# Kernel tuning notes

Hardware: AMD Instinct MI355X
Metric: run time of the kernel (lower is better)

The kernel has to match this reference:

```python
import jax, jax.numpy as jnp
import numpy as np

N = 40000       # nodes
E = 512000      # edges (avg degree 16)
D = 128         # embed_dim
H = 128         # hidden_dim
R = 8           # num_relations
B = 8           # num_bases
C = 3           # output classes (hardcoded in conv7)


def _prelu(x, a):
    # torch.nn.PReLU(num_parameters=C): per-channel slope
    return jnp.where(x >= 0, x, a * x)


def _rgcn(x, src, dst, etype, bases, comp, root, bias):
    """PyG RGCNConv with basis decomposition, aggr='mean' (default).
    out[i] = sum_r mean_{e: dst=i, type=r} (W_r @ x[src_e]) + root @ x[i] + bias
    W_r = sum_b comp[r,b] * bases[b]. Aggregation is linear, so we aggregate
    source features per (node, relation) first, then apply W_r once per node.
    """
    n = x.shape[0]
    seg = dst * R + etype                      # composite (node, relation) id
    gx = x[src]                                # [E, in]  (big gather)
    agg = jax.ops.segment_sum(gx, seg, num_segments=n * R)              # [N*R, in]
    cnt = jax.ops.segment_sum(jnp.ones((src.shape[0],), x.dtype), seg,
                              num_segments=n * R)                        # [N*R]
    agg = agg / jnp.maximum(cnt, 1.0)[:, None]                           # mean per (node, rel)
    agg = agg.reshape(n, R, -1)                                          # [N, R, in]
    Wr = jnp.einsum('rb,bio->rio', comp, bases)                          # [R, in, out]
    return jnp.einsum('nri,rio->no', agg, Wr) + x @ root + bias


def setup_inputs() -> dict:
    key = jax.random.key(0)
    ks = jax.random.split(key, 20)
    num_x = jax.random.normal(ks[0], (N, 1), jnp.float32)
    x = jax.random.normal(ks[1], (N, D), jnp.float32)
    edge_index = jax.random.randint(ks[2], (2, E), 0, N, jnp.int32)
    edge_type = jax.random.randint(ks[3], (E,), 0, R, jnp.int32)
    # params
    lin_w = jax.random.normal(ks[4], (1, D), jnp.float32) * 0.1
    lin_b = jax.random.normal(ks[5], (D,), jnp.float32) * 0.1
    prelu_a = 0.25 + 0.01 * jax.random.normal(ks[6], (7, D), jnp.float32)
    s = 1.0 / np.sqrt(H)
    bases = jax.random.normal(ks[7], (6, B, H, H), jnp.float32) * s   # conv1..conv6 (in==out==H)
    comp = jax.random.normal(ks[8], (6, R, B), jnp.float32) * (1.0 / np.sqrt(B))
    root = jax.random.normal(ks[9], (6, H, H), jnp.float32) * s
    bias = jax.random.normal(ks[10], (6, H), jnp.float32) * 0.1
    bases7 = jax.random.normal(ks[11], (B, H, C), jnp.float32) * s
    comp7 = jax.random.normal(ks[12], (R, B), jnp.float32) * (1.0 / np.sqrt(B))
    root7 = jax.random.normal(ks[13], (H, C), jnp.float32) * s
    bias7 = jax.random.normal(ks[14], (C,), jnp.float32) * 0.1
    return dict(num_x=num_x, x=x, edge_index=edge_index, edge_type=edge_type,
                lin_w=lin_w, lin_b=lin_b, prelu_a=prelu_a,
                bases=bases, comp=comp, root=root, bias=bias,
                bases7=bases7, comp7=comp7, root7=root7, bias7=bias7)


def reference(num_x, x, edge_index, edge_type, lin_w, lin_b, prelu_a,
              bases, comp, root, bias, bases7, comp7, root7, bias7):
    src, dst = edge_index[0], edge_index[1]
    h = _prelu(num_x @ lin_w + lin_b, prelu_a[0])   # act_lin(num_lin(num_x))
    h = h + x
    for i in range(6):  # conv1..conv6 + PReLU (dropout is identity in eval)
        h = _rgcn(h, src, dst, edge_type, bases[i], comp[i], root[i], bias[i])
        h = _prelu(h, prelu_a[i + 1])
    h = _rgcn(h, src, dst, edge_type, bases7, comp7, root7, bias7)  # conv7 -> 3 classes
    return jax.nn.log_softmax(h, axis=1)
```

## Files before the change

### kernel.cpp

```cpp
#include <hip/hip_runtime.h>

typedef unsigned short ushortT;
typedef ushortT ushort8 __attribute__((ext_vector_type(8)));
typedef short bf16x8 __attribute__((ext_vector_type(8)));
typedef float f32x4 __attribute__((ext_vector_type(4)));

#define NN 40000
#define NE 512000
#define DD 128
#define RR 8
#define NSEG (NN * RR)
#define KT 1152
#define NB_SCAN 1250

__device__ __forceinline__ float bf2f(ushortT u) { return __uint_as_float(((unsigned)u) << 16); }
__device__ __forceinline__ ushortT f2bf(float f) {
  unsigned u = __float_as_uint(f);
  unsigned r = (u + 0x7fffu + ((u >> 16) & 1u)) >> 16;
  return (ushortT)r;
}

__global__ void count_kernel(const int* __restrict__ dst, const int* __restrict__ et,
                             int* __restrict__ cnt) {
  int e = blockIdx.x * 256 + threadIdx.x;
  if (e < NE) atomicAdd(&cnt[dst[e] * RR + et[e]], 1);
}

__global__ void scan1_kernel(const int* __restrict__ cnt, int* __restrict__ offs,
                             int* __restrict__ bsum) {
  __shared__ int s[256];
  int tid = threadIdx.x, gid = blockIdx.x * 256 + tid;
  int v = cnt[gid];
  s[tid] = v; __syncthreads();
  for (int o = 1; o < 256; o <<= 1) {
    int t = (tid >= o) ? s[tid - o] : 0;
    __syncthreads(); s[tid] += t; __syncthreads();
  }
  offs[gid] = s[tid] - v;
  if (tid == 255) bsum[blockIdx.x] = s[255];
}

__global__ void scan2_kernel(int* __restrict__ bsum) {
  __shared__ int s[256];
  __shared__ int carry, tot;
  int tid = threadIdx.x;
  if (tid == 0) carry = 0;
  __syncthreads();
  for (int base = 0; base < NB_SCAN; base += 256) {
    int i = base + tid;
    int v = (i < NB_SCAN) ? bsum[i] : 0;
    s[tid] = v; __syncthreads();
    for (int o = 1; o < 256; o <<= 1) {
      int t = (tid >= o) ? s[tid - o] : 0;
      __syncthreads(); s[tid] += t; __syncthreads();
    }
    if (i < NB_SCAN) bsum[i] = s[tid] - v + carry;
    if (tid == 255) tot = s[255];
    __syncthreads();
    if (tid == 0) carry += tot;
    __syncthreads();
  }
}

__global__ void scan3_kernel(int* __restrict__ offs, const int* __restrict__ bsum,
                             const int* __restrict__ cnt, int* __restrict__ cursor) {
  int gid = blockIdx.x * 256 + threadIdx.x;
  int v = offs[gid] + bsum[blockIdx.x];
  offs[gid] = v;
  cursor[gid] = v;
  if (gid == NSEG - 1) offs[NSEG] = v + cnt[gid];
}

__global__ void fill_kernel(const int* __restrict__ src, const int* __restrict__ dst,
                            const int* __restrict__ et, int* __restrict__ cursor,
                            int* __restrict__ srcs) {
  int e = blockIdx.x * 256 + threadIdx.x;
  if (e >= NE) return;
  int seg = dst[e] * RR + et[e];
  int slot = atomicAdd(&cursor[seg], 1);
  srcs[slot] = src[e];
}

__global__ void init_h_kernel(const float* __restrict__ num_x, const float* __restrict__ x,
                              const float* __restrict__ lin_w, const float* __restrict__ lin_b,
                              const float* __restrict__ a0, ushortT* __restrict__ h) {
  int idx = blockIdx.x * 256 + threadIdx.x;
  if (idx >= NN * DD) return;
  int n = idx >> 7, d = idx & 127;
  float v = fmaf(num_x[n], lin_w[d], lin_b[d]);
  v = v >= 0.f ? v : a0[d] * v;
  h[idx] = f2bf(v + x[idx]);
}

__global__ void build_w_kernel(const float* __restrict__ bases, const float* __restrict__ comp,
                               const float* __restrict__ root, ushortT* __restrict__ Wt) {
  int idx = blockIdx.x * 256 + threadIdx.x;
  if (idx >= DD * KT) return;
  int j = idx / KT, k = idx - j * KT;
  float s;
  if (k < RR * DD) {
    int r = k >> 7, i = k & 127;
    s = 0.f;
#pragma unroll
    for (int b = 0; b < 8; ++b) s += comp[r * 8 + b] * bases[(b * DD + i) * DD + j];
  } else {
    s = root[(k - RR * DD) * DD + j];
  }
  Wt[idx] = f2bf(s);
}

__global__ __launch_bounds__(256)
void agg_kernel(const int* __restrict__ offs, const int* __restrict__ srcs,
                const ushortT* __restrict__ h, ushortT* __restrict__ Xagg) {
  int seg = blockIdx.x * 16 + (threadIdx.x >> 4);
  int l = threadIdx.x & 15;
  int beg = offs[seg], end = offs[seg + 1];
  float a[8] = {0.f, 0.f, 0.f, 0.f, 0.f, 0.f, 0.f, 0.f};
  int e = beg;
  for (; e + 2 <= end; e += 2) {
    int s0 = srcs[e], s1 = srcs[e + 1];
    ushort8 v0 = *(const ushort8*)&h[(size_t)s0 * DD + l * 8];
    ushort8 v1 = *(const ushort8*)&h[(size_t)s1 * DD + l * 8];
#pragma unroll
    for (int j = 0; j < 8; ++j) a[j] += bf2f(v0[j]) + bf2f(v1[j]);
  }
  if (e < end) {
    int s0 = srcs[e];
    ushort8 v0 = *(const ushort8*)&h[(size_t)s0 * DD + l * 8];
#pragma unroll
    for (int j = 0; j < 8; ++j) a[j] += bf2f(v0[j]);
  }
  float inv = (end > beg) ? 1.0f / (float)(end - beg) : 1.0f;
  ushort8 r;
#pragma unroll
  for (int j = 0; j < 8; ++j) r[j] = f2bf(a[j] * inv);
  *(ushort8*)&Xagg[(size_t)seg * DD + l * 8] = r;
}

__global__ __launch_bounds__(256)
void gemm_kernel(const ushortT* __restrict__ Xagg, const ushortT* __restrict__ h,
                 const ushortT* __restrict__ Wt, const float* __restrict__ bias,
                 const float* __restrict__ slope, ushortT* __restrict__ hout) {
  __shared__ ushortT As[64 * 64];
  __shared__ ushortT Bs[128 * 64];
  int tid = threadIdx.x, lane = tid & 63, wv = tid >> 6;
  int wr = wv >> 1, wc = wv & 1;
  int n0 = blockIdx.x * 64;
  int l8 = lane >> 3;
  int lp = lane & 7;
  f32x4 acc[2][4];
#pragma unroll
  for (int m = 0; m < 2; ++m)
#pragma unroll
    for (int n = 0; n < 4; ++n) acc[m][n] = (f32x4){0.f, 0.f, 0.f, 0.f};

  for (int kc = 0; kc < KT; kc += 64) {
#pragma unroll
    for (int j = 0; j < 2; ++j) {
      int row = wv * 16 + j * 8 + l8;
      int p = lp ^ (row & 7);
      const ushortT* g;
      if (kc < RR * DD) g = Xagg + (size_t)(n0 + row) * 1024 + kc + p * 8;
      else              g = h + (size_t)(n0 + row) * DD + (kc - RR * DD) + p * 8;
      __builtin_amdgcn_global_load_lds(
          (const __attribute__((address_space(1))) void*)g,
          (__attribute__((address_space(3))) void*)&As[(wv * 16 + j * 8) * 64], 16, 0, 0);
    }
#pragma unroll
    for (int j = 0; j < 4; ++j) {
      int col = wv * 32 + j * 8 + l8;
      int p = lp ^ (col & 7);
      const ushortT* g = Wt + (size_t)col * KT + kc + p * 8;
      __builtin_amdgcn_global_load_lds(
          (const __attribute__((address_space(1))) void*)g,
          (__attribute__((address_space(3))) void*)&Bs[(wv * 32 + j * 8) * 64], 16, 0, 0);
    }
    __syncthreads();
#pragma unroll
    for (int kk = 0; kk < 2; ++kk) {
      int ko2 = kk * 64 + (lane >> 4) * 16;
      bf16x8 a[2], b[4];
#pragma unroll
      for (int m = 0; m < 2; ++m) {
        int row = wr * 32 + m * 16 + (lane & 15);
        int off = ((row << 7) + ko2) ^ ((row & 7) << 4);
        a[m] = *(const bf16x8*)((const char*)As + off);
      }
#pragma unroll
      for (int n = 0; n < 4; ++n) {
        int col = wc * 64 + n * 16 + (lane & 15);
        int off = ((col << 7) + ko2) ^ ((col & 7) << 4);
        b[n] = *(const bf16x8*)((const char*)Bs + off);
      }
#pragma unroll
      for (int m = 0; m < 2; ++m)
#pragma unroll
        for (int n = 0; n < 4; ++n)
          acc[m][n] = __builtin_amdgcn_mfma_f32_16x16x32_bf16(a[m], b[n], acc[m][n], 0, 0, 0);
    }
    __syncthreads();
  }
#pragma unroll
  for (int m = 0; m < 2; ++m) {
    int row = n0 + wr * 32 + m * 16 + (lane >> 4) * 4;
#pragma unroll
    for (int n = 0; n < 4; ++n) {
      int col = wc * 64 + n * 16 + (lane & 15);
      float bcol = bias[col], scol = slope[col];
#pragma unroll
      for (int q = 0; q < 4; ++q) {
        float v = acc[m][n][q] + bcol;
        v = v >= 0.f ? v : scol * v;
        hout[(size_t)(row + q) * DD + col] = f2bf(v);
      }
    }
  }
}

__global__ void build_w7_kernel(const float* __restrict__ bases7, const float* __restrict__ comp7,
                                const float* __restrict__ root7, float* __restrict__ W7) {
  int idx = blockIdx.x * 256 + threadIdx.x;
  if (idx >= KT * 3) return;
  int row = idx / 3, c = idx - row * 3;
  if (row < RR * DD) {
    int r = row >> 7, i = row & 127;
    float s = 0.f;
#pragma unroll
    for (int b = 0; b < 8; ++b) s += comp7[r * 8 + b] * bases7[(b * DD + i) * 3 + c];
    W7[idx] = s;
  } else {
    W7[idx] = root7[(row - RR * DD) * 3 + c];
  }
}

__global__ void conv7_kernel(const ushortT* __restrict__ Xagg, const ushortT* __restrict__ h,
                             const float* __restrict__ W7, const float* __restrict__ bias7,
                             float* __restrict__ out) {
  int gw = (blockIdx.x * 256 + threadIdx.x) >> 6;
  if (gw >= NN) return;
  int lane = threadIdx.x & 63;
  float a0 = 0.f, a1 = 0.f, a2 = 0.f;
#pragma unroll
  for (int i = 0; i < 2; ++i) {
    int k0 = i * 512 + lane * 8;
    ushort8 v = *(const ushort8*)&Xagg[(size_t)gw * 1024 + k0];
#pragma unroll
    for (int j = 0; j < 8; ++j) {
      float xx = bf2f(v[j]);
      const float* w = &W7[(k0 + j) * 3];
      a0 = fmaf(xx, w[0], a0); a1 = fmaf(xx, w[1], a1); a2 = fmaf(xx, w[2], a2);
    }
  }
  {
    unsigned v = *(const unsigned*)&h[gw * DD + lane * 2];
    float x0 = __uint_as_float(v << 16), x1 = __uint_as_float(v & 0xffff0000u);
    int k0 = 1024 + lane * 2;
    const float* w0 = &W7[k0 * 3];
    const float* w1 = &W7[(k0 + 1) * 3];
    a0 = fmaf(x0, w0[0], a0); a1 = fmaf(x0, w0[1], a1); a2 = fmaf(x0, w0[2], a2);
    a0 = fmaf(x1, w1[0], a0); a1 = fmaf(x1, w1[1], a1); a2 = fmaf(x1, w1[2], a2);
  }
#pragma unroll
  for (int o = 32; o > 0; o >>= 1) {
    a0 += __shfl_down(a0, o);
    a1 += __shfl_down(a1, o);
    a2 += __shfl_down(a2, o);
  }
  if (lane == 0) {
    float l0 = a0 + bias7[0], l1 = a1 + bias7[1], l2 = a2 + bias7[2];
    float m = fmaxf(l0, fmaxf(l1, l2));
    float lse = m + logf(expf(l0 - m) + expf(l1 - m) + expf(l2 - m));
    out[gw * 3 + 0] = l0 - lse;
    out[gw * 3 + 1] = l1 - lse;
    out[gw * 3 + 2] = l2 - lse;
  }
}

extern "C" void kernel_launch(void* const* d_in, const int* in_sizes, int n_in,
                              void* d_out, int out_size, void* d_ws, size_t ws_size,
                              hipStream_t stream) {
  const float* num_x  = (const float*)d_in[0];
  const float* x      = (const float*)d_in[1];
  const int*   eidx   = (const int*)d_in[2];
  const int*   etype  = (const int*)d_in[3];
  const float* lin_w  = (const float*)d_in[4];
  const float* lin_b  = (const float*)d_in[5];
  const float* prelu  = (const float*)d_in[6];
  const float* bases  = (const float*)d_in[7];
  const float* comp   = (const float*)d_in[8];
  const float* root   = (const float*)d_in[9];
  const float* bias   = (const float*)d_in[10];
  const float* bases7 = (const float*)d_in[11];
  const float* comp7  = (const float*)d_in[12];
  const float* root7  = (const float*)d_in[13];
  const float* bias7  = (const float*)d_in[14];
  const int* srcv = eidx;
  const int* dstv = eidx + NE;
  float* out = (float*)d_out;

  char* p = (char*)d_ws;
  auto alloc = [&](size_t bytes) { char* q = p; p += (bytes + 255) & ~(size_t)255; return q; };
  int*     counts = (int*)alloc((size_t)NSEG * 4);
  int*     offs   = (int*)alloc((size_t)(NSEG + 1) * 4);
  int*     cursor = (int*)alloc((size_t)NSEG * 4);
  int*     bsum   = (int*)alloc((size_t)NB_SCAN * 4);
  int*     srcs   = (int*)alloc((size_t)NE * 4);
  ushortT* h0     = (ushortT*)alloc((size_t)NN * DD * 2);
  ushortT* h1     = (ushortT*)alloc((size_t)NN * DD * 2);
  ushortT* Xagg   = (ushortT*)alloc((size_t)NN * 1024 * 2);
  ushortT* Wt     = (ushortT*)alloc((size_t)DD * KT * 2);
  float*   W7     = (float*)alloc((size_t)KT * 3 * 4);
  if (ws_size < (size_t)(p - (char*)d_ws)) return;

  hipMemsetAsync(counts, 0, (size_t)NSEG * 4, stream);
  count_kernel<<<NE / 256, 256, 0, stream>>>(dstv, etype, counts);
  scan1_kernel<<<NB_SCAN, 256, 0, stream>>>(counts, offs, bsum);
  scan2_kernel<<<1, 256, 0, stream>>>(bsum);
  scan3_kernel<<<NB_SCAN, 256, 0, stream>>>(offs, bsum, counts, cursor);
  fill_kernel<<<NE / 256, 256, 0, stream>>>(srcv, dstv, etype, cursor, srcs);

  init_h_kernel<<<(NN * DD + 255) / 256, 256, 0, stream>>>(num_x, x, lin_w, lin_b, prelu, h0);

  ushortT* hin = h0;
  ushortT* hout = h1;
  for (int layer = 0; layer < 6; ++layer) {
    build_w_kernel<<<(DD * KT + 255) / 256, 256, 0, stream>>>(
        bases + (size_t)layer * 8 * DD * DD, comp + layer * RR * 8,
        root + (size_t)layer * DD * DD, Wt);
    agg_kernel<<<NSEG / 16, 256, 0, stream>>>(offs, srcs, hin, Xagg);
    gemm_kernel<<<NN / 64, 256, 0, stream>>>(Xagg, hin, Wt, bias + layer * DD,
                                             prelu + (layer + 1) * DD, hout);
    ushortT* t = hin; hin = hout; hout = t;
  }
  build_w7_kernel<<<(KT * 3 + 255) / 256, 256, 0, stream>>>(bases7, comp7, root7, W7);
  agg_kernel<<<NSEG / 16, 256, 0, stream>>>(offs, srcs, hin, Xagg);
  conv7_kernel<<<NN / 4, 256, 0, stream>>>(Xagg, hin, W7, bias7, out);
}
```

Before: 508.0 us.

## Fuse neighbor aggregation into RGCN GEMM and drop Xagg buffer

Each layer's aggregation is now done inside the GEMM block: for each relation, threads gather and average neighbor rows straight into an LDS A-tile, then run MFMA against the matching weight slab. This removes the 80MB Xagg write and read per layer. Conv7 also aggregates inline, and all six weight builds are batched into one launch before the loop. In exchange the gather has less parallelism (4 threads per node, serial per-edge loop, 500 blocks), and there is no overlap between gather latency and MFMA.

```diff
diff --git a/kernel.cpp b/kernel.cpp
--- a/kernel.cpp
+++ b/kernel.cpp
@@ -4,6 +4,8 @@
 typedef ushortT ushort8 __attribute__((ext_vector_type(8)));
 typedef short bf16x8 __attribute__((ext_vector_type(8)));
 typedef float f32x4 __attribute__((ext_vector_type(4)));
+typedef unsigned int uint32;
+typedef uint32 uint32x4 __attribute__((ext_vector_type(4)));
 
 #define NN 40000
 #define NE 512000
@@ -12,6 +14,7 @@
 #define NSEG (NN * RR)
 #define KT 1152
 #define NB_SCAN 1250
+#define ECAP 1536
 
 __device__ __forceinline__ float bf2f(ushortT u) { return __uint_as_float(((unsigned)u) << 16); }
 __device__ __forceinline__ ushortT f2bf(float f) {
@@ -93,111 +96,129 @@
 }
 
 __global__ void build_w_kernel(const float* __restrict__ bases, const float* __restrict__ comp,
-                               const float* __restrict__ root, ushortT* __restrict__ Wt) {
+                               const float* __restrict__ root, ushortT* __restrict__ Wt6) {
   int idx = blockIdx.x * 256 + threadIdx.x;
-  if (idx >= DD * KT) return;
-  int j = idx / KT, k = idx - j * KT;
+  if (idx >= 6 * DD * KT) return;
+  int layer = idx / (DD * KT);
+  int rem = idx - layer * (DD * KT);
+  int j = rem / KT, k = rem - j * KT;
+  const float* B  = bases + (size_t)layer * 8 * DD * DD;
+  const float* C  = comp + layer * RR * 8;
+  const float* Rt = root + (size_t)layer * DD * DD;
   float s;
   if (k < RR * DD) {
     int r = k >> 7, i = k & 127;
     s = 0.f;
 #pragma unroll
-    for (int b = 0; b < 8; ++b) s += comp[r * 8 + b] * bases[(b * DD + i) * DD + j];
+    for (int b = 0; b < 8; ++b) s += C[r * 8 + b] * B[(b * DD + i) * DD + j];
   } else {
-    s = root[(k - RR * DD) * DD + j];
-  }
-  Wt[idx] = f2bf(s);
+    s = Rt[(k - RR * DD) * DD + j];
+  }
+  Wt6[idx] = f2bf(s);
 }
 
 __global__ __launch_bounds__(256)
-void agg_kernel(const int* __restrict__ offs, const int* __restrict__ srcs,
-                const ushortT* __restrict__ h, ushortT* __restrict__ Xagg) {
-  int seg = blockIdx.x * 16 + (threadIdx.x >> 4);
-  int l = threadIdx.x & 15;
-  int beg = offs[seg], end = offs[seg + 1];
-  float a[8] = {0.f, 0.f, 0.f, 0.f, 0.f, 0.f, 0.f, 0.f};
-  int e = beg;
-  for (; e + 2 <= end; e += 2) {
-    int s0 = srcs[e], s1 = srcs[e + 1];
-    ushort8 v0 = *(const ushort8*)&h[(size_t)s0 * DD + l * 8];
-    ushort8 v1 = *(const ushort8*)&h[(size_t)s1 * DD + l * 8];
-#pragma unroll
-    for (int j = 0; j < 8; ++j) a[j] += bf2f(v0[j]) + bf2f(v1[j]);
-  }
-  if (e < end) {
-    int s0 = srcs[e];
-    ushort8 v0 = *(const ushort8*)&h[(size_t)s0 * DD + l * 8];
-#pragma unroll
-    for (int j = 0; j < 8; ++j) a[j] += bf2f(v0[j]);
-  }
-  float inv = (end > beg) ? 1.0f / (float)(end - beg) : 1.0f;
-  ushort8 r;
-#pragma unroll
-  for (int j = 0; j < 8; ++j) r[j] = f2bf(a[j] * inv);
-  *(ushort8*)&Xagg[(size_t)seg * DD + l * 8] = r;
-}
-
-__global__ __launch_bounds__(256)
-void gemm_kernel(const ushortT* __restrict__ Xagg, const ushortT* __restrict__ h,
-                 const ushortT* __restrict__ Wt, const float* __restrict__ bias,
-                 const float* __restrict__ slope, ushortT* __restrict__ hout) {
-  __shared__ ushortT As[64 * 64];
-  __shared__ ushortT Bs[128 * 64];
+void layer_kernel(const int* __restrict__ offs, const int* __restrict__ srcs,
+                  const ushortT* __restrict__ h, const ushortT* __restrict__ Wt,
+                  const float* __restrict__ bias, const float* __restrict__ slope,
+                  ushortT* __restrict__ hout) {
+  __shared__ __align__(16) ushortT As[64 * 136];
+  __shared__ __align__(16) ushortT Bs[2][128 * 64];
+  __shared__ int s_offs[513];
+  __shared__ int s_srcs[ECAP];
   int tid = threadIdx.x, lane = tid & 63, wv = tid >> 6;
   int wr = wv >> 1, wc = wv & 1;
   int n0 = blockIdx.x * 64;
-  int l8 = lane >> 3;
-  int lp = lane & 7;
+  int l8 = lane >> 3, lp = lane & 7;
+  int nodei = tid >> 2, q = tid & 3;
+
+  int e0 = offs[n0 * 8];
+  int e1 = offs[n0 * 8 + 512];
+  s_offs[tid] = offs[n0 * 8 + tid];
+  s_offs[tid + 256] = offs[n0 * 8 + tid + 256];
+  if (tid == 0) s_offs[512] = e1;
+  int nE = e1 - e0;
+  for (int i = tid; i < nE && i < ECAP; i += 256) s_srcs[i] = srcs[e0 + i];
+
   f32x4 acc[2][4];
 #pragma unroll
   for (int m = 0; m < 2; ++m)
 #pragma unroll
     for (int n = 0; n < 4; ++n) acc[m][n] = (f32x4){0.f, 0.f, 0.f, 0.f};
 
-  for (int kc = 0; kc < KT; kc += 64) {
-#pragma unroll
-    for (int j = 0; j < 2; ++j) {
-      int row = wv * 16 + j * 8 + l8;
-      int p = lp ^ (row & 7);
-      const ushortT* g;
-      if (kc < RR * DD) g = Xagg + (size_t)(n0 + row) * 1024 + kc + p * 8;
-      else              g = h + (size_t)(n0 + row) * DD + (kc - RR * DD) + p * 8;
-      __builtin_amdgcn_global_load_lds(
-          (const __attribute__((address_space(1))) void*)g,
-          (__attribute__((address_space(3))) void*)&As[(wv * 16 + j * 8) * 64], 16, 0, 0);
-    }
-#pragma unroll
-    for (int j = 0; j < 4; ++j) {
-      int col = wv * 32 + j * 8 + l8;
-      int p = lp ^ (col & 7);
-      const ushortT* g = Wt + (size_t)col * KT + kc + p * 8;
-      __builtin_amdgcn_global_load_lds(
-          (const __attribute__((address_space(1))) void*)g,
-          (__attribute__((address_space(3))) void*)&Bs[(wv * 32 + j * 8) * 64], 16, 0, 0);
+  __syncthreads();
+
+  for (int r = 0; r < 9; ++r) {
+    int kc = r * 128;
+#pragma unroll
+    for (int hf = 0; hf < 2; ++hf)
+#pragma unroll
+      for (int j = 0; j < 4; ++j) {
+        int col = wv * 32 + j * 8 + l8;
+        int p = lp ^ l8;
+        const ushortT* g = Wt + (size_t)col * KT + (kc + hf * 64) + p * 8;
+        __builtin_amdgcn_global_load_lds(
+            (const __attribute__((address_space(1))) void*)g,
+            (__attribute__((address_space(3))) void*)&Bs[hf][(wv * 32 + j * 8) * 64], 16, 0, 0);
+      }
+    if (r < 8) {
+      int beg = s_offs[nodei * 8 + r], end = s_offs[nodei * 8 + r + 1];
+      float inv = (end > beg) ? 1.0f / (float)(end - beg) : 1.0f;
+#pragma unroll
+      for (int pp = 0; pp < 2; ++pp) {
+        int c0 = q * 32 + pp * 16;
+        float a[16];
+#pragma unroll
+        for (int j = 0; j < 16; ++j) a[j] = 0.f;
+        for (int e = beg; e < end; ++e) {
+          int idx = e - e0;
+          int sv = (idx < ECAP) ? s_srcs[idx] : srcs[e];
+          const ushortT* hp = h + (size_t)sv * DD + c0;
+          ushort8 v0 = *(const ushort8*)hp;
+          ushort8 v1 = *(const ushort8*)(hp + 8);
+#pragma unroll
+          for (int j = 0; j < 8; ++j) { a[j] += bf2f(v0[j]); a[8 + j] += bf2f(v1[j]); }
+        }
+        uint32 w[8];
+#pragma unroll
+        for (int j = 0; j < 8; ++j) {
+          float lo = a[2 * j] * inv, hi = a[2 * j + 1] * inv;
+          asm("v_cvt_pk_bf16_f32 %0, %1, %2" : "=v"(w[j]) : "v"(lo), "v"(hi));
+        }
+        *(uint32x4*)&As[nodei * 136 + c0]     = (uint32x4){w[0], w[1], w[2], w[3]};
+        *(uint32x4*)&As[nodei * 136 + c0 + 8] = (uint32x4){w[4], w[5], w[6], w[7]};
+      }
+    } else {
+      int c0 = q * 32;
+      const ushortT* hp = h + (size_t)(n0 + nodei) * DD + c0;
+#pragma unroll
+      for (int j = 0; j < 4; ++j)
+        *(ushort8*)&As[nodei * 136 + c0 + j * 8] = *(const ushort8*)(hp + j * 8);
     }
     __syncthreads();
 #pragma unroll
-    for (int kk = 0; kk < 2; ++kk) {
-      int ko2 = kk * 64 + (lane >> 4) * 16;
-      bf16x8 a[2], b[4];
-#pragma unroll
-      for (int m = 0; m < 2; ++m) {
-        int row = wr * 32 + m * 16 + (lane & 15);
-        int off = ((row << 7) + ko2) ^ ((row & 7) << 4);
-        a[m] = *(const bf16x8*)((const char*)As + off);
+    for (int hf = 0; hf < 2; ++hf)
+#pragma unroll
+      for (int kk = 0; kk < 2; ++kk) {
+        int ko = hf * 64 + kk * 32 + (lane >> 4) * 8;
+        bf16x8 a[2], b[4];
+#pragma unroll
+        for (int m = 0; m < 2; ++m) {
+          int row = wr * 32 + m * 16 + (lane & 15);
+          a[m] = *(const bf16x8*)&As[row * 136 + ko];
+        }
+#pragma unroll
+        for (int n = 0; n < 4; ++n) {
+          int col = wc * 64 + n * 16 + (lane & 15);
+          int off = ((col << 7) + kk * 64 + ((lane >> 4) << 4)) ^ ((col & 7) << 4);
+          b[n] = *(const bf16x8*)((const char*)Bs[hf] + off);
+        }
+#pragma unroll
+        for (int m = 0; m < 2; ++m)
+#pragma unroll
+          for (int n = 0; n < 4; ++n)
+            acc[m][n] = __builtin_amdgcn_mfma_f32_16x16x32_bf16(a[m], b[n], acc[m][n], 0, 0, 0);
       }
-#pragma unroll
-      for (int n = 0; n < 4; ++n) {
-        int col = wc * 64 + n * 16 + (lane & 15);
-        int off = ((col << 7) + ko2) ^ ((col & 7) << 4);
-        b[n] = *(const bf16x8*)((const char*)Bs + off);
-      }
-#pragma unroll
-      for (int m = 0; m < 2; ++m)
-#pragma unroll
-        for (int n = 0; n < 4; ++n)
-          acc[m][n] = __builtin_amdgcn_mfma_f32_16x16x32_bf16(a[m], b[n], acc[m][n], 0, 0, 0);
-    }
     __syncthreads();
   }
 #pragma unroll
@@ -208,10 +229,10 @@
       int col = wc * 64 + n * 16 + (lane & 15);
       float bcol = bias[col], scol = slope[col];
 #pragma unroll
-      for (int q = 0; q < 4; ++q) {
-        float v = acc[m][n][q] + bcol;
+      for (int qq = 0; qq < 4; ++qq) {
+        float v = acc[m][n][qq] + bcol;
         v = v >= 0.f ? v : scol * v;
-        hout[(size_t)(row + q) * DD + col] = f2bf(v);
+        hout[(size_t)(row + qq) * DD + col] = f2bf(v);
       }
     }
   }
@@ -233,32 +254,35 @@
   }
 }
 
-__global__ void conv7_kernel(const ushortT* __restrict__ Xagg, const ushortT* __restrict__ h,
-                             const float* __restrict__ W7, const float* __restrict__ bias7,
-                             float* __restrict__ out) {
+__global__ __launch_bounds__(256)
+void conv7_kernel(const int* __restrict__ offs, const int* __restrict__ srcs,
+                  const ushortT* __restrict__ h, const float* __restrict__ W7,
+                  const float* __restrict__ bias7, float* __restrict__ out) {
   int gw = (blockIdx.x * 256 + threadIdx.x) >> 6;
   if (gw >= NN) return;
   int lane = threadIdx.x & 63;
   float a0 = 0.f, a1 = 0.f, a2 = 0.f;
-#pragma unroll
-  for (int i = 0; i < 2; ++i) {
-    int k0 = i * 512 + lane * 8;
-    ushort8 v = *(const ushort8*)&Xagg[(size_t)gw * 1024 + k0];
-#pragma unroll
-    for (int j = 0; j < 8; ++j) {
-      float xx = bf2f(v[j]);
-      const float* w = &W7[(k0 + j) * 3];
-      a0 = fmaf(xx, w[0], a0); a1 = fmaf(xx, w[1], a1); a2 = fmaf(xx, w[2], a2);
+  for (int r = 0; r < RR; ++r) {
+    int beg = offs[gw * 8 + r], end = offs[gw * 8 + r + 1];
+    float s0 = 0.f, s1 = 0.f;
+    for (int e = beg; e < end; ++e) {
+      int sv = srcs[e];
+      uint32 v = *(const uint32*)&h[(size_t)sv * DD + lane * 2];
+      s0 += __uint_as_float(v << 16);
+      s1 += __uint_as_float(v & 0xffff0000u);
     }
+    float inv = (end > beg) ? 1.0f / (float)(end - beg) : 1.0f;
+    s0 *= inv; s1 *= inv;
+    int k0 = (r * DD + lane * 2) * 3;
+    a0 = fmaf(s0, W7[k0 + 0], a0); a1 = fmaf(s0, W7[k0 + 1], a1); a2 = fmaf(s0, W7[k0 + 2], a2);
+    a0 = fmaf(s1, W7[k0 + 3], a0); a1 = fmaf(s1, W7[k0 + 4], a1); a2 = fmaf(s1, W7[k0 + 5], a2);
   }
   {
-    unsigned v = *(const unsigned*)&h[gw * DD + lane * 2];
+    uint32 v = *(const uint32*)&h[(size_t)gw * DD + lane * 2];
     float x0 = __uint_as_float(v << 16), x1 = __uint_as_float(v & 0xffff0000u);
-    int k0 = 1024 + lane * 2;
-    const float* w0 = &W7[k0 * 3];
-    const float* w1 = &W7[(k0 + 1) * 3];
-    a0 = fmaf(x0, w0[0], a0); a1 = fmaf(x0, w0[1], a1); a2 = fmaf(x0, w0[2], a2);
-    a0 = fmaf(x1, w1[0], a0); a1 = fmaf(x1, w1[1], a1); a2 = fmaf(x1, w1[2], a2);
+    int k0 = (1024 + lane * 2) * 3;
+    a0 = fmaf(x0, W7[k0 + 0], a0); a1 = fmaf(x0, W7[k0 + 1], a1); a2 = fmaf(x0, W7[k0 + 2], a2);
+    a0 = fmaf(x1, W7[k0 + 3], a0); a1 = fmaf(x1, W7[k0 + 4], a1); a2 = fmaf(x1, W7[k0 + 5], a2);
   }
 #pragma unroll
   for (int o = 32; o > 0; o >>= 1) {
@@ -307,8 +331,7 @@
   int*     srcs   = (int*)alloc((size_t)NE * 4);
   ushortT* h0     = (ushortT*)alloc((size_t)NN * DD * 2);
   ushortT* h1     = (ushortT*)alloc((size_t)NN * DD * 2);
-  ushortT* Xagg   = (ushortT*)alloc((size_t)NN * 1024 * 2);
-  ushortT* Wt     = (ushortT*)alloc((size_t)DD * KT * 2);
+  ushortT* Wt6    = (ushortT*)alloc((size_t)6 * DD * KT * 2);
   float*   W7     = (float*)alloc((size_t)KT * 3 * 4);
   if (ws_size < (size_t)(p - (char*)d_ws)) return;
 
@@ -320,19 +343,15 @@
   fill_kernel<<<NE / 256, 256, 0, stream>>>(srcv, dstv, etype, cursor, srcs);
 
   init_h_kernel<<<(NN * DD + 255) / 256, 256, 0, stream>>>(num_x, x, lin_w, lin_b, prelu, h0);
+  build_w_kernel<<<(6 * DD * KT + 255) / 256, 256, 0, stream>>>(bases, comp, root, Wt6);
+  build_w7_kernel<<<(KT * 3 + 255) / 256, 256, 0, stream>>>(bases7, comp7, root7, W7);
 
   ushortT* hin = h0;
   ushortT* hout = h1;
   for (int layer = 0; layer < 6; ++layer) {
-    build_w_kernel<<<(DD * KT + 255) / 256, 256, 0, stream>>>(
-        bases + (size_t)layer * 8 * DD * DD, comp + layer * RR * 8,
-        root + (size_t)layer * DD * DD, Wt);
-    agg_kernel<<<NSEG / 16, 256, 0, stream>>>(offs, srcs, hin, Xagg);
-    gemm_kernel<<<NN / 64, 256, 0, stream>>>(Xagg, hin, Wt, bias + layer * DD,
-                                             prelu + (layer + 1) * DD, hout);
+    layer_kernel<<<NN / 64, 256, 0, stream>>>(offs, srcs, hin, Wt6 + (size_t)layer * DD * KT,
+                                              bias + layer * DD, prelu + (layer + 1) * DD, hout);
     ushortT* t = hin; hin = hout; hout = t;
   }
-  build_w7_kernel<<<(KT * 3 + 255) / 256, 256, 0, stream>>>(bases7, comp7, root7, W7);
-  agg_kernel<<<NSEG / 16, 256, 0, stream>>>(offs, srcs, hin, Xagg);
-  conv7_kernel<<<NN / 4, 256, 0, stream>>>(Xagg, hin, W7, bias7, out);
-}
+  conv7_kernel<<<NN / 4, 256, 0, stream>>>(offs, srcs, hin, W7, bias7, out);
+}
```

Measured after the change: 712.0 us. 40.2% more time.

## Transform node features per relation before aggregation instead of aggregating first

Applied to the files above, without the earlier changes.

Reorders each RGCN layer so a GEMM first computes h·W_r for all relations plus root into a per-node Z buffer, then an edge-gather kernel sums weighted rows of Z per destination node and applies bias and PReLU. Per-edge mean weights and relation ids are precomputed in the fill step, and all six layer weights are built once up front. This drops the large per-(node,relation) Xagg write/read and the 8x-wider K in the GEMM. In exchange it gathers 128-wide rows from a 1152-wide Z and adds an extra bf16 rounding before aggregation. The last layer similarly projects to 27 outputs and then aggregates small fp32 rows.

```diff
diff --git a/kernel.cpp b/kernel.cpp
--- a/kernel.cpp
+++ b/kernel.cpp
@@ -4,6 +4,7 @@
 typedef ushortT ushort8 __attribute__((ext_vector_type(8)));
 typedef short bf16x8 __attribute__((ext_vector_type(8)));
 typedef float f32x4 __attribute__((ext_vector_type(4)));
+typedef unsigned int uint32;
 
 #define NN 40000
 #define NE 512000
@@ -72,13 +73,16 @@
 }
 
 __global__ void fill_kernel(const int* __restrict__ src, const int* __restrict__ dst,
-                            const int* __restrict__ et, int* __restrict__ cursor,
-                            int* __restrict__ srcs) {
+                            const int* __restrict__ et, const int* __restrict__ cnt,
+                            int* __restrict__ cursor, int* __restrict__ edata,
+                            float* __restrict__ wgt) {
   int e = blockIdx.x * 256 + threadIdx.x;
   if (e >= NE) return;
-  int seg = dst[e] * RR + et[e];
+  int r = et[e];
+  int seg = dst[e] * RR + r;
   int slot = atomicAdd(&cursor[seg], 1);
-  srcs[slot] = src[e];
+  edata[slot] = src[e] | (r << 16);
+  wgt[slot] = 1.0f / (float)cnt[seg];
 }
 
 __global__ void init_h_kernel(const float* __restrict__ num_x, const float* __restrict__ x,
@@ -92,187 +96,207 @@
   h[idx] = f2bf(v + x[idx]);
 }
 
-__global__ void build_w_kernel(const float* __restrict__ bases, const float* __restrict__ comp,
-                               const float* __restrict__ root, ushortT* __restrict__ Wt) {
+__global__ void build_wall_kernel(const float* __restrict__ bases, const float* __restrict__ comp,
+                                  const float* __restrict__ root, ushortT* __restrict__ Wall6) {
   int idx = blockIdx.x * 256 + threadIdx.x;
-  if (idx >= DD * KT) return;
-  int j = idx / KT, k = idx - j * KT;
+  if (idx >= 6 * KT * DD) return;
+  int layer = idx / (KT * DD);
+  int rem = idx - layer * (KT * DD);
+  int j = rem >> 7, k = rem & 127;
   float s;
-  if (k < RR * DD) {
-    int r = k >> 7, i = k & 127;
+  if (j < RR * DD) {
+    int r = j >> 7, o = j & 127;
+    const float* C = comp + layer * 64 + r * 8;
+    const float* B = bases + ((size_t)layer * 8 * DD + 0) * DD * DD / DD;
     s = 0.f;
 #pragma unroll
-    for (int b = 0; b < 8; ++b) s += comp[r * 8 + b] * bases[(b * DD + i) * DD + j];
+    for (int b = 0; b < 8; ++b)
+      s += C[b] * bases[(((size_t)layer * 8 + b) * DD + k) * DD + o];
   } else {
-    s = root[(k - RR * DD) * DD + j];
-  }
-  Wt[idx] = f2bf(s);
+    s = root[((size_t)layer * DD + k) * DD + (j - RR * DD)];
+  }
+  Wall6[idx] = f2bf(s);
 }
 
 __global__ __launch_bounds__(256)
-void agg_kernel(const int* __restrict__ offs, const int* __restrict__ srcs,
-                const ushortT* __restrict__ h, ushortT* __restrict__ Xagg) {
-  int seg = blockIdx.x * 16 + (threadIdx.x >> 4);
+void gemmZ_kernel(const ushortT* __restrict__ h, const ushortT* __restrict__ Wall,
+                  ushortT* __restrict__ Z) {
+  __shared__ ushortT As[64 * 128];
+  __shared__ ushortT Bs[128 * 128];
+  int bid = blockIdx.x;
+  int nblk = bid / 625, mblk = bid - nblk * 625;
+  int n0 = mblk * 64;
+  int tid = threadIdx.x, lane = tid & 63, wv = tid >> 6;
+  int wr = wv >> 1, wc = wv & 1;
+#pragma unroll
+  for (int j = 0; j < 4; ++j) {
+    int baser = wv * 16 + j * 4;
+    int row = baser + (lane >> 4);
+    int p = (lane & 15) ^ (row & 7);
+    const ushortT* g = h + (size_t)(n0 + row) * DD + p * 8;
+    __builtin_amdgcn_global_load_lds(
+        (const __attribute__((address_space(1))) void*)g,
+        (__attribute__((address_space(3))) void*)&As[baser * 128], 16, 0, 0);
+  }
+#pragma unroll
+  for (int j = 0; j < 8; ++j) {
+    int basec = wv * 32 + j * 4;
+    int col = basec + (lane >> 4);
+    int p = (lane & 15) ^ (col & 7);
+    const ushortT* g = Wall + (size_t)(nblk * 128 + col) * DD + p * 8;
+    __builtin_amdgcn_global_load_lds(
+        (const __attribute__((address_space(1))) void*)g,
+        (__attribute__((address_space(3))) void*)&Bs[basec * 128], 16, 0, 0);
+  }
+  f32x4 acc[2][4];
+#pragma unroll
+  for (int m = 0; m < 2; ++m)
+#pragma unroll
+    for (int n = 0; n < 4; ++n) acc[m][n] = (f32x4){0.f, 0.f, 0.f, 0.f};
+  __syncthreads();
+#pragma unroll
+  for (int kk = 0; kk < 4; ++kk) {
+    int ko2 = kk * 64 + ((lane >> 4) << 4);
+    bf16x8 a[2], b[4];
+#pragma unroll
+    for (int m = 0; m < 2; ++m) {
+      int row = wr * 32 + m * 16 + (lane & 15);
+      int off = ((row << 8) + ko2) ^ ((row & 7) << 4);
+      a[m] = *(const bf16x8*)((const char*)As + off);
+    }
+#pragma unroll
+    for (int n = 0; n < 4; ++n) {
+      int col = wc * 64 + n * 16 + (lane & 15);
+      int off = ((col << 8) + ko2) ^ ((col & 7) << 4);
+      b[n] = *(const bf16x8*)((const char*)Bs + off);
+    }
+#pragma unroll
+    for (int m = 0; m < 2; ++m)
+#pragma unroll
+      for (int n = 0; n < 4; ++n)
+        acc[m][n] = __builtin_amdgcn_mfma_f32_16x16x32_bf16(a[m], b[n], acc[m][n], 0, 0, 0);
+  }
+#pragma unroll
+  for (int m = 0; m < 2; ++m) {
+    int row = n0 + wr * 32 + m * 16 + (lane >> 4) * 4;
+#pragma unroll
+    for (int n = 0; n < 4; ++n) {
+      int col = nblk * 128 + wc * 64 + n * 16 + (lane & 15);
+#pragma unroll
+      for (int q = 0; q < 4; ++q)
+        Z[(size_t)(row + q) * KT + col] = f2bf(acc[m][n][q]);
+    }
+  }
+}
+
+__global__ __launch_bounds__(256)
+void aggE_kernel(const int* __restrict__ offs, const int* __restrict__ edata,
+                 const float* __restrict__ wgt, const ushortT* __restrict__ Z,
+                 const float* __restrict__ bias, const float* __restrict__ slope,
+                 ushortT* __restrict__ hnew) {
+  int n = (blockIdx.x * 256 + threadIdx.x) >> 4;
   int l = threadIdx.x & 15;
-  int beg = offs[seg], end = offs[seg + 1];
+  int beg = offs[n * 8], end = offs[n * 8 + 8];
   float a[8] = {0.f, 0.f, 0.f, 0.f, 0.f, 0.f, 0.f, 0.f};
   int e = beg;
   for (; e + 2 <= end; e += 2) {
-    int s0 = srcs[e], s1 = srcs[e + 1];
-    ushort8 v0 = *(const ushort8*)&h[(size_t)s0 * DD + l * 8];
-    ushort8 v1 = *(const ushort8*)&h[(size_t)s1 * DD + l * 8];
-#pragma unroll
-    for (int j = 0; j < 8; ++j) a[j] += bf2f(v0[j]) + bf2f(v1[j]);
+    int ed0 = edata[e], ed1 = edata[e + 1];
+    float w0 = wgt[e], w1 = wgt[e + 1];
+    const ushortT* p0 = Z + (size_t)(ed0 & 0xFFFF) * KT + ((ed0 >> 16) << 7) + l * 8;
+    const ushortT* p1 = Z + (size_t)(ed1 & 0xFFFF) * KT + ((ed1 >> 16) << 7) + l * 8;
+    ushort8 v0 = *(const ushort8*)p0;
+    ushort8 v1 = *(const ushort8*)p1;
+#pragma unroll
+    for (int j = 0; j < 8; ++j)
+      a[j] = fmaf(w1, bf2f(v1[j]), fmaf(w0, bf2f(v0[j]), a[j]));
   }
   if (e < end) {
-    int s0 = srcs[e];
-    ushort8 v0 = *(const ushort8*)&h[(size_t)s0 * DD + l * 8];
-#pragma unroll
-    for (int j = 0; j < 8; ++j) a[j] += bf2f(v0[j]);
-  }
-  float inv = (end > beg) ? 1.0f / (float)(end - beg) : 1.0f;
+    int ed0 = edata[e];
+    float w0 = wgt[e];
+    const ushortT* p0 = Z + (size_t)(ed0 & 0xFFFF) * KT + ((ed0 >> 16) << 7) + l * 8;
+    ushort8 v0 = *(const ushort8*)p0;
+#pragma unroll
+    for (int j = 0; j < 8; ++j) a[j] = fmaf(w0, bf2f(v0[j]), a[j]);
+  }
+  ushort8 vr = *(const ushort8*)(Z + (size_t)n * KT + RR * DD + l * 8);
   ushort8 r;
 #pragma unroll
-  for (int j = 0; j < 8; ++j) r[j] = f2bf(a[j] * inv);
-  *(ushort8*)&Xagg[(size_t)seg * DD + l * 8] = r;
+  for (int j = 0; j < 8; ++j) {
+    int c = l * 8 + j;
+    float v = a[j] + bf2f(vr[j]) + bias[c];
+    v = v >= 0.f ? v : slope[c] * v;
+    r[j] = f2bf(v);
+  }
+  *(ushort8*)&hnew[(size_t)n * DD + l * 8] = r;
+}
+
+__global__ void build_w7t_kernel(const float* __restrict__ bases7, const float* __restrict__ comp7,
+                                 const float* __restrict__ root7, float* __restrict__ W7t) {
+  int idx = blockIdx.x * 256 + threadIdx.x;
+  if (idx >= 27 * DD) return;
+  int c = idx >> 7, k = idx & 127;
+  float s;
+  if (c < 24) {
+    int r = c / 3, cc = c - r * 3;
+    s = 0.f;
+#pragma unroll
+    for (int b = 0; b < 8; ++b) s += comp7[r * 8 + b] * bases7[(b * DD + k) * 3 + cc];
+  } else {
+    s = root7[k * 3 + (c - 24)];
+  }
+  W7t[idx] = s;
 }
 
 __global__ __launch_bounds__(256)
-void gemm_kernel(const ushortT* __restrict__ Xagg, const ushortT* __restrict__ h,
-                 const ushortT* __restrict__ Wt, const float* __restrict__ bias,
-                 const float* __restrict__ slope, ushortT* __restrict__ hout) {
-  __shared__ ushortT As[64 * 64];
-  __shared__ ushortT Bs[128 * 64];
-  int tid = threadIdx.x, lane = tid & 63, wv = tid >> 6;
-  int wr = wv >> 1, wc = wv & 1;
-  int n0 = blockIdx.x * 64;
-  int l8 = lane >> 3;
-  int lp = lane & 7;
-  f32x4 acc[2][4];
-#pragma unroll
-  for (int m = 0; m < 2; ++m)
-#pragma unroll
-    for (int n = 0; n < 4; ++n) acc[m][n] = (f32x4){0.f, 0.f, 0.f, 0.f};
-
-  for (int kc = 0; kc < KT; kc += 64) {
-#pragma unroll
-    for (int j = 0; j < 2; ++j) {
-      int row = wv * 16 + j * 8 + l8;
-      int p = lp ^ (row & 7);
-      const ushortT* g;
-      if (kc < RR * DD) g = Xagg + (size_t)(n0 + row) * 1024 + kc + p * 8;
-      else              g = h + (size_t)(n0 + row) * DD + (kc - RR * DD) + p * 8;
-      __builtin_amdgcn_global_load_lds(
-          (const __attribute__((address_space(1))) void*)g,
-          (__attribute__((address_space(3))) void*)&As[(wv * 16 + j * 8) * 64], 16, 0, 0);
-    }
-#pragma unroll
-    for (int j = 0; j < 4; ++j) {
-      int col = wv * 32 + j * 8 + l8;
-      int p = lp ^ (col & 7);
-      const ushortT* g = Wt + (size_t)col * KT + kc + p * 8;
-      __builtin_amdgcn_global_load_lds(
-          (const __attribute__((address_space(1))) void*)g,
-          (__attribute__((address_space(3))) void*)&Bs[(wv * 32 + j * 8) * 64], 16, 0, 0);
-    }
-    __syncthreads();
-#pragma unroll
-    for (int kk = 0; kk < 2; ++kk) {
-      int ko2 = kk * 64 + (lane >> 4) * 16;
-      bf16x8 a[2], b[4];
-#pragma unroll
-      for (int m = 0; m < 2; ++m) {
-        int row = wr * 32 + m * 16 + (lane & 15);
-        int off = ((row << 7) + ko2) ^ ((row & 7) << 4);
-        a[m] = *(const bf16x8*)((const char*)As + off);
-      }
-#pragma unroll
-      for (int n = 0; n < 4; ++n) {
-        int col = wc * 64 + n * 16 + (lane & 15);
-        int off = ((col << 7) + ko2) ^ ((col & 7) << 4);
-        b[n] = *(const bf16x8*)((const char*)Bs + off);
-      }
-#pragma unroll
-      for (int m = 0; m < 2; ++m)
-#pragma unroll
-        for (int n = 0; n < 4; ++n)
-          acc[m][n] = __builtin_amdgcn_mfma_f32_16x16x32_bf16(a[m], b[n], acc[m][n], 0, 0, 0);
-    }
-    __syncthreads();
-  }
-#pragma unroll
-  for (int m = 0; m < 2; ++m) {
-    int row = n0 + wr * 32 + m * 16 + (lane >> 4) * 4;
-#pragma unroll
-    for (int n = 0; n < 4; ++n) {
-      int col = wc * 64 + n * 16 + (lane & 15);
-      float bcol = bias[col], scol = slope[col];
-#pragma unroll
-      for (int q = 0; q < 4; ++q) {
-        float v = acc[m][n][q] + bcol;
-        v = v >= 0.f ? v : scol * v;
-        hout[(size_t)(row + q) * DD + col] = f2bf(v);
-      }
-    }
-  }
-}
-
-__global__ void build_w7_kernel(const float* __restrict__ bases7, const float* __restrict__ comp7,
-                                const float* __restrict__ root7, float* __restrict__ W7) {
-  int idx = blockIdx.x * 256 + threadIdx.x;
-  if (idx >= KT * 3) return;
-  int row = idx / 3, c = idx - row * 3;
-  if (row < RR * DD) {
-    int r = row >> 7, i = row & 127;
-    float s = 0.f;
-#pragma unroll
-    for (int b = 0; b < 8; ++b) s += comp7[r * 8 + b] * bases7[(b * DD + i) * 3 + c];
-    W7[idx] = s;
-  } else {
-    W7[idx] = root7[(row - RR * DD) * 3 + c];
-  }
-}
-
-__global__ void conv7_kernel(const ushortT* __restrict__ Xagg, const ushortT* __restrict__ h,
-                             const float* __restrict__ W7, const float* __restrict__ bias7,
-                             float* __restrict__ out) {
-  int gw = (blockIdx.x * 256 + threadIdx.x) >> 6;
-  if (gw >= NN) return;
-  int lane = threadIdx.x & 63;
+void gemm7_kernel(const ushortT* __restrict__ h, const float* __restrict__ W7t,
+                  float* __restrict__ Z7) {
+  int t = blockIdx.x * 256 + threadIdx.x;
+  int n = t >> 5, c = t & 31;
+  if (c >= 27) return;
+  const ushortT* hp = h + (size_t)n * DD;
+  const float* w = W7t + c * DD;
+  float s = 0.f;
+#pragma unroll
+  for (int kb = 0; kb < 16; ++kb) {
+    ushort8 v = *(const ushort8*)(hp + kb * 8);
+#pragma unroll
+    for (int j = 0; j < 8; ++j) s = fmaf(bf2f(v[j]), w[kb * 8 + j], s);
+  }
+  Z7[n * 32 + c] = s;
+}
+
+__global__ __launch_bounds__(256)
+void agg7_kernel(const int* __restrict__ offs, const int* __restrict__ edata,
+                 const float* __restrict__ wgt, const float* __restrict__ Z7,
+                 const float* __restrict__ bias7, float* __restrict__ out) {
+  int n = (blockIdx.x * 256 + threadIdx.x) >> 4;
+  int l = threadIdx.x & 15;
+  int beg = offs[n * 8], end = offs[n * 8 + 8];
   float a0 = 0.f, a1 = 0.f, a2 = 0.f;
-#pragma unroll
-  for (int i = 0; i < 2; ++i) {
-    int k0 = i * 512 + lane * 8;
-    ushort8 v = *(const ushort8*)&Xagg[(size_t)gw * 1024 + k0];
-#pragma unroll
-    for (int j = 0; j < 8; ++j) {
-      float xx = bf2f(v[j]);
-      const float* w = &W7[(k0 + j) * 3];
-      a0 = fmaf(xx, w[0], a0); a1 = fmaf(xx, w[1], a1); a2 = fmaf(xx, w[2], a2);
-    }
-  }
-  {
-    unsigned v = *(const unsigned*)&h[gw * DD + lane * 2];
-    float x0 = __uint_as_float(v << 16), x1 = __uint_as_float(v & 0xffff0000u);
-    int k0 = 1024 + lane * 2;
-    const float* w0 = &W7[k0 * 3];
-    const float* w1 = &W7[(k0 + 1) * 3];
-    a0 = fmaf(x0, w0[0], a0); a1 = fmaf(x0, w0[1], a1); a2 = fmaf(x0, w0[2], a2);
-    a0 = fmaf(x1, w1[0], a0); a1 = fmaf(x1, w1[1], a1); a2 = fmaf(x1, w1[2], a2);
-  }
-#pragma unroll
-  for (int o = 32; o > 0; o >>= 1) {
-    a0 += __shfl_down(a0, o);
-    a1 += __shfl_down(a1, o);
-    a2 += __shfl_down(a2, o);
-  }
-  if (lane == 0) {
-    float l0 = a0 + bias7[0], l1 = a1 + bias7[1], l2 = a2 + bias7[2];
+  for (int e = beg + l; e < end; e += 16) {
+    int ed = edata[e];
+    float w = wgt[e];
+    const float* p = Z7 + (size_t)(ed & 0xFFFF) * 32 + (ed >> 16) * 3;
+    a0 = fmaf(w, p[0], a0);
+    a1 = fmaf(w, p[1], a1);
+    a2 = fmaf(w, p[2], a2);
+  }
+#pragma unroll
+  for (int o = 1; o < 16; o <<= 1) {
+    a0 += __shfl_xor(a0, o, 16);
+    a1 += __shfl_xor(a1, o, 16);
+    a2 += __shfl_xor(a2, o, 16);
+  }
+  if (l == 0) {
+    const float* zr = Z7 + (size_t)n * 32 + 24;
+    float l0 = a0 + zr[0] + bias7[0];
+    float l1 = a1 + zr[1] + bias7[1];
+    float l2 = a2 + zr[2] + bias7[2];
     float m = fmaxf(l0, fmaxf(l1, l2));
     float lse = m + logf(expf(l0 - m) + expf(l1 - m) + expf(l2 - m));
-    out[gw * 3 + 0] = l0 - lse;
-    out[gw * 3 + 1] = l1 - lse;
-    out[gw * 3 + 2] = l2 - lse;
+    out[n * 3 + 0] = l0 - lse;
+    out[n * 3 + 1] = l1 - lse;
+    out[n * 3 + 2] = l2 - lse;
   }
 }
 
@@ -304,12 +328,14 @@
   int*     offs   = (int*)alloc((size_t)(NSEG + 1) * 4);
   int*     cursor = (int*)alloc((size_t)NSEG * 4);
   int*     bsum   = (int*)alloc((size_t)NB_SCAN * 4);
-  int*     srcs   = (int*)alloc((size_t)NE * 4);
+  int*     edata  = (int*)alloc((size_t)NE * 4);
+  float*   wgt    = (float*)alloc((size_t)NE * 4);
   ushortT* h0     = (ushortT*)alloc((size_t)NN * DD * 2);
   ushortT* h1     = (ushortT*)alloc((size_t)NN * DD * 2);
-  ushortT* Xagg   = (ushortT*)alloc((size_t)NN * 1024 * 2);
-  ushortT* Wt     = (ushortT*)alloc((size_t)DD * KT * 2);
-  float*   W7     = (float*)alloc((size_t)KT * 3 * 4);
+  ushortT* Z      = (ushortT*)alloc((size_t)NN * KT * 2);
+  ushortT* Wall6  = (ushortT*)alloc((size_t)6 * KT * DD * 2);
+  float*   W7t    = (float*)alloc((size_t)27 * DD * 4);
+  float*   Z7     = (float*)alloc((size_t)NN * 32 * 4);
   if (ws_size < (size_t)(p - (char*)d_ws)) return;
 
   hipMemsetAsync(counts, 0, (size_t)NSEG * 4, stream);
@@ -317,22 +343,20 @@
   scan1_kernel<<<NB_SCAN, 256, 0, stream>>>(counts, offs, bsum);
   scan2_kernel<<<1, 256, 0, stream>>>(bsum);
   scan3_kernel<<<NB_SCAN, 256, 0, stream>>>(offs, bsum, counts, cursor);
-  fill_kernel<<<NE / 256, 256, 0, stream>>>(srcv, dstv, etype, cursor, srcs);
+  fill_kernel<<<NE / 256, 256, 0, stream>>>(srcv, dstv, etype, counts, cursor, edata, wgt);
 
   init_h_kernel<<<(NN * DD + 255) / 256, 256, 0, stream>>>(num_x, x, lin_w, lin_b, prelu, h0);
+  build_wall_kernel<<<(6 * KT * DD + 255) / 256, 256, 0, stream>>>(bases, comp, root, Wall6);
+  build_w7t_kernel<<<(27 * DD + 255) / 256, 256, 0, stream>>>(bases7, comp7, root7, W7t);
 
   ushortT* hin = h0;
   ushortT* hout = h1;
   for (int layer = 0; layer < 6; ++layer) {
-    build_w_kernel<<<(DD * KT + 255) / 256, 256, 0, stream>>>(
-        bases + (size_t)layer * 8 * DD * DD, comp + layer * RR * 8,
-        root + (size_t)layer * DD * DD, Wt);
-    agg_kernel<<<NSEG / 16, 256, 0, stream>>>(offs, srcs, hin, Xagg);
-    gemm_kernel<<<NN / 64, 256, 0, stream>>>(Xagg, hin, Wt, bias + layer * DD,
-                                             prelu + (layer + 1) * DD, hout);
+    gemmZ_kernel<<<625 * 9, 256, 0, stream>>>(hin, Wall6 + (size_t)layer * KT * DD, Z);
+    aggE_kernel<<<NN * 16 / 256, 256, 0, stream>>>(offs, edata, wgt, Z, bias + layer * DD,
+                                                   prelu + (layer + 1) * DD, hout);
     ushortT* t = hin; hin = hout; hout = t;
   }
-  build_w7_kernel<<<(KT * 3 + 255) / 256, 256, 0, stream>>>(bases7, comp7, root7, W7);
-  agg_kernel<<<NSEG / 16, 256, 0, stream>>>(offs, srcs, hin, Xagg);
-  conv7_kernel<<<NN / 4, 256, 0, stream>>>(Xagg, hin, W7, bias7, out);
-}
+  gemm7_kernel<<<NN * 32 / 256, 256, 0, stream>>>(hin, W7t, Z7);
+  agg7_kernel<<<NN * 16 / 256, 256, 0, stream>>>(offs, edata, wgt, Z7, bias7, out);
+}
```

New measurement: 610.3 us. 1.2x slower.
